# Kernel tuning notes

Measured on AMD Instinct MI355X. Metric: run time of the kernel, lower is better.

## Reference

```python
import jax, jax.numpy as jnp
import numpy as np

N_SAMPLES = 2 ** 15          # 32768
STEP = 256                   # transform_step_size
WIN = 2048                   # transform/synthesis window
N_FRAMES = N_SAMPLES // STEP # 128
N_COEFFS = WIN // 2 + 1      # 1025
DILATIONS = (1, 2, 4, 8, 16, 32, 64, 1)


def hann(n):
    return 0.5 - 0.5 * jnp.cos(2.0 * jnp.pi * jnp.arange(n, dtype=jnp.float32) / n)


def transform(audio):
    # audio: (B, 1, N) -> magnitude STFT (B, 1024, 128)
    x = audio[:, 0, :]
    x = jnp.pad(x, ((0, 0), (0, WIN - STEP)))  # pad so n_frames == N_SAMPLES // STEP
    idx = np.arange(N_FRAMES)[:, None] * STEP + np.arange(WIN)[None, :]
    frames = x[:, idx] * hann(WIN)
    spec = jnp.abs(jnp.fft.rfft(frames, norm='ortho'))   # (B, F, 1025)
    return spec[..., : N_COEFFS - 1].transpose(0, 2, 1)  # (B, 1024, F)


def conv1x1(x, w, b):
    # x: (B, I, T), w: (O, I, 1), b: (O,)
    return jnp.einsum('oi,bit->bot', w[:, :, 0], x) + b[None, :, None]


def anticausal_block(x, w, b, dilation):
    # kernel_size=2 anti-causal dilated conv: looks at t and t+dilation (pad future)
    x_fut = jnp.pad(x, ((0, 0), (0, 0), (0, dilation)))[:, :, dilation:]
    y = (jnp.einsum('oi,bit->bot', w[:, :, 0], x)
         + jnp.einsum('oi,bit->bot', w[:, :, 1], x_fut)
         + b[None, :, None])
    y = jax.nn.leaky_relu(y, 0.2)
    y = y + x
    # do_norm: per-example max-norm
    y = y / (jnp.max(jnp.abs(y), axis=(1, 2), keepdims=True) + 1e-8)
    return y


def upsample_with_holes(x, desired_size):
    # zero-stuffing upsample: out[..., ::step] = x
    b, c, t = x.shape
    step = desired_size // t
    out = jnp.zeros((b, c, desired_size), x.dtype)
    return out.at[:, :, ::step].set(x)


def freq_domain_resonance(coeffs):
    # coeffs: (1, C, 1025) in [0, 1); per-frame decay = repeated spectral multiply
    c = jnp.clip(coeffs, 0.0, 0.9999)
    exps = jnp.arange(1, N_FRAMES + 1, dtype=coeffs.dtype)
    mags = c[:, :, None, :] ** exps[None, None, :, None]     # (1, C, F, 1025)
    frames = jnp.fft.irfft(mags, n=WIN) * hann(WIN)
    hop = WIN // 2
    total = hop * (N_FRAMES - 1) + WIN
    idx = np.arange(N_FRAMES)[:, None] * hop + np.arange(WIN)[None, :]
    out = jnp.zeros(frames.shape[:2] + (total,), frames.dtype)
    out = out.at[:, :, idx].add(frames)                      # overlap-add
    return out[..., :N_SAMPLES]                              # (1, C, N)


def fft_convolve(a, b):
    # circular-free conv via zero-padding to 2N, keep first N (matches repo fft_convolve)
    n = a.shape[-1]
    spec = jnp.fft.rfft(a, n=2 * n) * jnp.fft.rfft(b, n=2 * n)
    return jnp.fft.irfft(spec, n=2 * n)[..., :n]


def reference(audio, proj_in_w, proj_in_b, blocks_w, blocks_b,
              proj_sparse_w, proj_sparse_b, proj_dense_w, proj_dense_b, resonances):
    spec = transform(audio)                         # (B, 1024, 128)
    h = conv1x1(spec, proj_in_w, proj_in_b)         # (B, 32, 128)
    acc = jnp.zeros_like(h)
    for i, d in enumerate(DILATIONS):               # fixed 8-block stack
        h = anticausal_block(h, blocks_w[i], blocks_b[i], d)
        acc = acc + h
    x = conv1x1(acc, proj_sparse_w, proj_sparse_b)  # (B, 256, 128)
    sparse = jax.nn.relu(x)
    x = conv1x1(sparse, proj_dense_w, proj_dense_b) # (B, 32, 128)
    x = upsample_with_holes(x, N_SAMPLES)           # (B, 32, 32768)
    res = freq_domain_resonance(resonances)         # (1, 32, 32768), broadcast over B
    y = fft_convolve(x, res)                        # (B, 32, 32768)
    y = jnp.sum(y, axis=1, keepdims=True)           # (B, 1, 32768)
    return y, sparse


def setup_inputs() -> dict:
    key = jax.random.key(0)
    ks = jax.random.split(key, 12)
    u = lambda k, shape: jax.random.uniform(k, shape, jnp.float32, -0.05, 0.05)
    return {
        'audio': jax.random.normal(ks[0], (32, 1, N_SAMPLES), jnp.float32),
        'proj_in_w': u(ks[1], (32, 1024, 1)),
        'proj_in_b': jnp.zeros((32,), jnp.float32),
        'blocks_w': u(ks[2], (8, 32, 32, 2)),
        'blocks_b': jnp.zeros((8, 32), jnp.float32),
        'proj_sparse_w': u(ks[3], (256, 32, 1)),
        'proj_sparse_b': jnp.zeros((256,), jnp.float32),
        'proj_dense_w': u(ks[4], (32, 256, 1)),
        'proj_dense_b': jnp.zeros((32,), jnp.float32),
        'resonances': jax.random.uniform(ks[5], (1, 32, N_COEFFS), jnp.float32, 0.0, 1.0),
    }
```

## Files before the change

### kernel.cpp

```cpp
#include <hip/hip_runtime.h>

#define PI_F 3.14159265358979323846f

typedef short bf16x8 __attribute__((ext_vector_type(8)));
typedef float f32x4 __attribute__((ext_vector_type(4)));

#define MFMA16(acc, a, b) \
  acc = __builtin_amdgcn_mfma_f32_16x16x32_bf16(a, b, acc, 0, 0, 0)

#define WS_SPEC   0u
#define WS_H0     4194304u
#define WS_ACC    4325376u
#define WS_V      4456448u
#define WS_WTIN   4587520u
#define WS_WST    4620288u
#define WS_WDT    4628480u
#define WS_FRAMES 4636672u
#define WS_RES    6733824u

#define BIX(a) ((a) + ((a) >> 4))

#define BFLY(I0, I1, C, S)                                   \
  { float2 u = buf[I0]; float2 w = buf[I1];                  \
    float tr = (C) * w.x - (S) * w.y;                        \
    float ti = (C) * w.y + (S) * w.x;                        \
    buf[I0] = make_float2(u.x + tr, u.y + ti);               \
    buf[I1] = make_float2(u.x - tr, u.y - ti); }

__device__ __forceinline__ void quad_bfly(float2* buf, int a, int h,
                                          float cs, float ss, float cp, float sp) {
  float2 x0 = buf[BIX(a)],         x1 = buf[BIX(a + h)];
  float2 x2 = buf[BIX(a + 2 * h)], x3 = buf[BIX(a + 3 * h)];
  float t1x = cs * x1.x - ss * x1.y, t1y = cs * x1.y + ss * x1.x;
  float t3x = cs * x3.x - ss * x3.y, t3y = cs * x3.y + ss * x3.x;
  float2 y0 = make_float2(x0.x + t1x, x0.y + t1y);
  float2 y1 = make_float2(x0.x - t1x, x0.y - t1y);
  float2 y2 = make_float2(x2.x + t3x, x2.y + t3y);
  float2 y3 = make_float2(x2.x - t3x, x2.y - t3y);
  float u2x = cp * y2.x - sp * y2.y, u2y = cp * y2.y + sp * y2.x;
  float u3x = sp * y3.x + cp * y3.y, u3y = sp * y3.y - cp * y3.x;
  buf[BIX(a)]         = make_float2(y0.x + u2x, y0.y + u2y);
  buf[BIX(a + 2 * h)] = make_float2(y0.x - u2x, y0.y - u2y);
  buf[BIX(a + h)]     = make_float2(y1.x + u3x, y1.y + u3y);
  buf[BIX(a + 3 * h)] = make_float2(y1.x - u3x, y1.y - u3y);
}

__device__ __forceinline__ void fft2048_stages(float2* buf, int tid) {
  const float R = 0.7071067811865476f;
  for (int g = tid; g < 512; g += 256) {
    int a = g << 2;
    float2 x0 = buf[BIX(a)],     x1 = buf[BIX(a + 1)];
    float2 x2 = buf[BIX(a + 2)], x3 = buf[BIX(a + 3)];
    float2 y0 = make_float2(x0.x + x1.x, x0.y + x1.y);
    float2 y1 = make_float2(x0.x - x1.x, x0.y - x1.y);
    float2 y2 = make_float2(x2.x + x3.x, x2.y + x3.y);
    float2 y3 = make_float2(x2.x - x3.x, x2.y - x3.y);
    buf[BIX(a)]     = make_float2(y0.x + y2.x, y0.y + y2.y);
    buf[BIX(a + 2)] = make_float2(y0.x - y2.x, y0.y - y2.y);
    buf[BIX(a + 1)] = make_float2(y1.x + y3.y, y1.y - y3.x);
    buf[BIX(a + 3)] = make_float2(y1.x - y3.y, y1.y + y3.x);
  }
  __syncthreads();
  {
    int j = tid & 3;
    const float C8 = 0.9238795325112867f, S8 = 0.3826834323650898f;
    float cs = (j == 0) ? 1.f : ((j == 1) ? R : ((j == 2) ? 0.f : -R));
    float ss = (j == 0) ? 0.f : ((j == 2) ? -1.f : -R);
    float cp = (j == 0) ? 1.f : ((j == 1) ? C8 : ((j == 2) ? R : S8));
    float sp = (j == 0) ? 0.f : ((j == 1) ? -S8 : ((j == 2) ? -R : -C8));
    for (int g = tid; g < 512; g += 256) {
      int a = ((g >> 2) << 4) + j;
      quad_bfly(buf, a, 4, cs, ss, cp, sp);
    }
  }
  __syncthreads();
#pragma unroll
  for (int s = 4; s <= 8; s += 2) {
    int h = 1 << s;
    int j = tid & (h - 1);
    float ss, cs, sp, cp;
    __sincosf(-PI_F / (float)h * (float)j, &ss, &cs);
    __sincosf(-PI_F / (float)(2 * h) * (float)j, &sp, &cp);
    for (int g = tid; g < 512; g += 256) {
      int a = ((g >> s) << (s + 2)) + j;
      quad_bfly(buf, a, h, cs, ss, cp, sp);
    }
    __syncthreads();
  }
  {
    float s0, c0;
    __sincosf(-PI_F / 1024.f * (float)tid, &s0, &c0);
    BFLY(BIX(tid),       BIX(tid + 1024), c0, s0);
    BFLY(BIX(tid + 256), BIX(tid + 1280), R * (c0 + s0), R * (s0 - c0));
    BFLY(BIX(tid + 512), BIX(tid + 1536), s0, -c0);
    BFLY(BIX(tid + 768), BIX(tid + 1792), R * (s0 - c0), -R * (s0 + c0));
  }
  __syncthreads();
}

__global__ __launch_bounds__(256) void k_fft(const float* __restrict__ audio,
                                             const float* __restrict__ resin,
                                             const float* __restrict__ Win,
                                             const float* __restrict__ Ws,
                                             const float* __restrict__ Wd,
                                             const float* __restrict__ bwIn,
                                             float* __restrict__ spec,
                                             float* __restrict__ frames,
                                             float* __restrict__ WT,
                                             float* __restrict__ WsT,
                                             float* __restrict__ WdT,
                                             short* __restrict__ Whg,
                                             short* __restrict__ Wlg) {
  __shared__ float2 buf[2176];
  int blk = blockIdx.x;

  if (blk >= 2560) {
    int i = (blk - 2560) * 256 + threadIdx.x;
    if (i < 32768) { int o = i >> 10, k = i & 1023; WT[k * 32 + o] = Win[i]; }
    if (i < 8192)  { int o2 = i >> 5, m = i & 31;   WsT[m * 256 + o2] = Ws[i]; }
    if (i < 8192)  { int c = i >> 8, o2 = i & 255;  WdT[o2 * 32 + c] = Wd[i]; }
    if (i < 16384) {
      int w = i & 1, m = (i >> 1) & 31, o = (i >> 6) & 31, s = i >> 11;
      float val = bwIn[i];
      unsigned bits = __float_as_uint(val);
      float rem = val - __uint_as_float(bits & 0xffff0000u);
      int row = (s * 2 + w) * 32 + o;
      Whg[row * 32 + m] = (short)(bits >> 16);
      Wlg[row * 32 + m] = (short)(__float_as_uint(rem) >> 16);
    }
    return;
  }

  if (blk < 2048) {
    int b  = blk >> 6;
    int f0 = (blk & 63) * 2;
    for (int j = threadIdx.x; j < 2048; j += 256) {
      float h = 0.5f - 0.5f * __cosf(0.0030679615757712823f * (float)j);
      int i1 = f0 * 256 + j;
      int i2 = i1 + 256;
      float a1 = (i1 < 32768) ? audio[b * 32768 + i1] : 0.f;
      float a2 = (i2 < 32768) ? audio[b * 32768 + i2] : 0.f;
      buf[BIX(__brev((unsigned)j) >> 21)] = make_float2(a1 * h, a2 * h);
    }
    __syncthreads();
    fft2048_stages(buf, threadIdx.x);
    const float scale = 0.5f * 0.022097086912079608f;
    for (int k = threadIdx.x; k < 1024; k += 256) {
      float2 zk = buf[BIX(k)];
      float2 zn = buf[BIX((2048 - k) & 2047)];
      float f1r = zk.x + zn.x, f1i = zk.y - zn.y;
      float f2r = zk.y + zn.y, f2i = zk.x - zn.x;
      spec[(b * 128 + f0) * 1024 + k]     = sqrtf(f1r * f1r + f1i * f1i) * scale;
      spec[(b * 128 + f0 + 1) * 1024 + k] = sqrtf(f2r * f2r + f2i * f2i) * scale;
    }
  } else {
    int r = blk - 2048;
    int c = r >> 4;
    int g = r & 15;
    float e1 = (float)(2 * g + 1);
    for (int k = threadIdx.x; k < 2048; k += 256) {
      int kk = (k <= 1024) ? k : 2048 - k;
      float cv = resin[c * 1025 + kk];
      cv = fminf(fmaxf(cv, 0.f), 0.9999f);
      float m1 = __powf(cv, e1);
      float m2 = m1 * cv;
      buf[BIX(__brev((unsigned)k) >> 21)] = make_float2(m1, m2);
    }
    __syncthreads();
    fft2048_stages(buf, threadIdx.x);
    for (int j = threadIdx.x; j < 2048; j += 256) {
      float h  = 0.5f - 0.5f * __cosf(0.0030679615757712823f * (float)j);
      float sc = h * (1.f / 2048.f);
      float2 z = buf[BIX(j)];
      frames[(c * 32 + 2 * g) * 2048 + j]     = z.x * sc;
      frames[(c * 32 + 2 * g + 1) * 2048 + j] = z.y * sc;
    }
  }
}

__global__ __launch_bounds__(256) void k_proj_in(const float* __restrict__ spec,
                                                 const float* __restrict__ WT,
                                                 const float* __restrict__ bias,
                                                 float* __restrict__ h0) {
  __shared__ float specL[8][1024];
  __shared__ float red[32][8][8];
  int b  = blockIdx.x >> 4;
  int t0 = (blockIdx.x & 15) * 8;
  for (int i = threadIdx.x; i < 8192; i += 256) {
    int tt = i >> 10, k = i & 1023;
    specL[tt][k] = spec[(b * 128 + t0 + tt) * 1024 + k];
  }
  __syncthreads();
  int o = threadIdx.x & 31, p = threadIdx.x >> 5;
  float part[8] = {0.f,0.f,0.f,0.f,0.f,0.f,0.f,0.f};
  for (int i = 0; i < 128; ++i) {
    int k = p * 128 + ((i + p * 4) & 127);
    float w = WT[k * 32 + o];
#pragma unroll
    for (int tt = 0; tt < 8; ++tt) part[tt] += w * specL[tt][k];
  }
#pragma unroll
  for (int tt = 0; tt < 8; ++tt) red[o][tt][p] = part[tt];
  __syncthreads();
  int oo = threadIdx.x >> 3, tt2 = threadIdx.x & 7;
  float s = bias[oo];
#pragma unroll
  for (int p2 = 0; p2 < 8; ++p2) s += red[oo][tt2][p2];
  h0[b * 4096 + oo * 128 + t0 + tt2] = s;
}

__global__ __launch_bounds__(256) void k_obpack(const float* __restrict__ frames,
                                                short* __restrict__ Bh,
                                                short* __restrict__ Bl) {
  int c = blockIdx.x >> 4, o = blockIdx.x & 15;
  int r = threadIdx.x;
  bf16x8 hv, lv;
#pragma unroll
  for (int j = 0; j < 8; ++j) {
    int fo = 8 * o + j;
    int g  = fo >> 2;
    int j0 = ((fo & 3) << 8) + r;
    float val = frames[(c * 32 + g) * 2048 + j0];
    if (g > 0) val += frames[(c * 32 + g - 1) * 2048 + j0 + 1024];
    unsigned bits = __float_as_uint(val);
    float rem = val - __uint_as_float(bits & 0xffff0000u);
    hv[j] = (short)(bits >> 16);
    lv[j] = (short)(__float_as_uint(rem) >> 16);
  }
  int unit = (blockIdx.x * 16 + (r >> 4)) * 16 + (r & 15);
  ((bf16x8*)Bh)[unit] = hv;
  ((bf16x8*)Bl)[unit] = lv;
}

__global__ __launch_bounds__(1024) void k_chain(const float* __restrict__ h0,
                                                const short* __restrict__ Whg,
                                                const short* __restrict__ Wlg,
                                                const float* __restrict__ bb,
                                                float* __restrict__ accout) {
  __shared__ __align__(16) short Hh[192 * 40];
  __shared__ __align__(16) short Hl[192 * 40];
  __shared__ float Hf[128 * 33];
  __shared__ float bL[256];
  __shared__ float red[16];
  int b = blockIdx.x, tid = threadIdx.x;

  for (int i = tid; i < 4096; i += 1024) {
    int t = i & 127;
    int o = i >> 7;
    float val = h0[b * 4096 + i];
    Hf[t * 33 + o] = val;
    unsigned bits = __float_as_uint(val);
    float rem = val - __uint_as_float(bits & 0xffff0000u);
    Hh[t * 40 + o] = (short)(bits >> 16);
    Hl[t * 40 + o] = (short)(__float_as_uint(rem) >> 16);
  }
  for (int i = tid; i < 64 * 40; i += 1024) {
    Hh[128 * 40 + i] = 0;
    Hl[128 * 40 + i] = 0;
  }
  if (tid < 256) bL[tid] = bb[tid];
  __syncthreads();

  int wave = tid >> 6, lane = tid & 63;
  int quad = lane >> 4, l15 = lane & 15;
  int t0 = (wave & 7) * 16, o0 = (wave >> 3) * 16;
  int tD = t0 + quad * 4;
  int oD = o0 + l15;

  const bf16x8* Hh8 = (const bf16x8*)Hh;
  const bf16x8* Hl8 = (const bf16x8*)Hl;
  const bf16x8* Wh8 = (const bf16x8*)Whg;
  const bf16x8* Wl8 = (const bf16x8*)Wlg;

  float accsum[4] = {0.f, 0.f, 0.f, 0.f};
  const int DIL[8] = {1, 2, 4, 8, 16, 32, 64, 1};

#pragma unroll
  for (int s = 0; s < 8; ++s) {
    int arow = t0 + l15;
    int frow = arow + DIL[s];
    bf16x8 Ah = Hh8[arow * 5 + quad];
    bf16x8 Al = Hl8[arow * 5 + quad];
    bf16x8 Fh = Hh8[frow * 5 + quad];
    bf16x8 Fl = Hl8[frow * 5 + quad];
    int w0row = ((s * 2 + 0) * 32 + oD) * 4 + quad;
    int w1row = ((s * 2 + 1) * 32 + oD) * 4 + quad;
    bf16x8 B0h = Wh8[w0row], B0l = Wl8[w0row];
    bf16x8 B1h = Wh8[w1row], B1l = Wl8[w1row];
    float bias = bL[s * 32 + oD];
    f32x4 acc = {bias, bias, bias, bias};
    MFMA16(acc, Ah, B0h); MFMA16(acc, Ah, B0l); MFMA16(acc, Al, B0h);
    MFMA16(acc, Fh, B1h); MFMA16(acc, Fh, B1l); MFMA16(acc, Fl, B1h);
    float hnew[4], lmax = 0.f;
#pragma unroll
    for (int r = 0; r < 4; ++r) {
      float sv = acc[r];
      sv = (sv > 0.f) ? sv : 0.2f * sv;
      sv += Hf[(tD + r) * 33 + oD];
      hnew[r] = sv;
      lmax = fmaxf(lmax, fabsf(sv));
    }
#pragma unroll
    for (int off = 32; off > 0; off >>= 1)
      lmax = fmaxf(lmax, __shfl_down(lmax, off, 64));
    if (lane == 0) red[wave] = lmax;
    __syncthreads();
    float mx = red[0];
#pragma unroll
    for (int i = 1; i < 16; ++i) mx = fmaxf(mx, red[i]);
    float nm = 1.f / (mx + 1e-8f);
#pragma unroll
    for (int r = 0; r < 4; ++r) {
      float hv = hnew[r] * nm;
      accsum[r] += hv;
      int t = tD + r;
      Hf[t * 33 + oD] = hv;
      unsigned bits = __float_as_uint(hv);
      float rem = hv - __uint_as_float(bits & 0xffff0000u);
      Hh[t * 40 + oD] = (short)(bits >> 16);
      Hl[t * 40 + oD] = (short)(__float_as_uint(rem) >> 16);
    }
    __syncthreads();
  }
#pragma unroll
  for (int r = 0; r < 4; ++r)
    accout[b * 4096 + (tD + r) * 32 + oD] = accsum[r];
}

__global__ __launch_bounds__(256) void k_sparse_dense(const float* __restrict__ acc,
                                                      const float* __restrict__ WsT,
                                                      const float* __restrict__ bs,
                                                      const float* __restrict__ WdT,
                                                      const float* __restrict__ bd,
                                                      float* __restrict__ out_sparse,
                                                      float* __restrict__ v) {
  __shared__ float accL[4][32];
  __shared__ float sL[4][256];
  __shared__ float red[8][4][32];
  int b = blockIdx.x >> 5, tq = blockIdx.x & 31;
  int t0 = tq * 4;
  int tid = threadIdx.x;
  if (tid < 128)
    accL[tid >> 5][tid & 31] = acc[b * 4096 + (t0 + (tid >> 5)) * 32 + (tid & 31)];
  __syncthreads();
  float bsv = bs[tid];
  float s0 = bsv, s1 = bsv, s2 = bsv, s3 = bsv;
  for (int m = 0; m < 32; ++m) {
    float w = WsT[m * 256 + tid];
    s0 += w * accL[0][m]; s1 += w * accL[1][m];
    s2 += w * accL[2][m]; s3 += w * accL[3][m];
  }
  s0 = fmaxf(s0, 0.f); s1 = fmaxf(s1, 0.f); s2 = fmaxf(s2, 0.f); s3 = fmaxf(s3, 0.f);
  float* os = out_sparse + b * 32768 + tid * 128 + t0;
  os[0] = s0; os[1] = s1; os[2] = s2; os[3] = s3;
  sL[0][tid] = s0; sL[1][tid] = s1; sL[2][tid] = s2; sL[3][tid] = s3;
  __syncthreads();
  int c = tid & 31, p = tid >> 5;
  float p0 = 0.f, p1 = 0.f, p2 = 0.f, p3 = 0.f;
  for (int jj = 0; jj < 32; ++jj) {
    int o2 = p * 32 + jj;
    float w = WdT[o2 * 32 + c];
    p0 += w * sL[0][o2]; p1 += w * sL[1][o2];
    p2 += w * sL[2][o2]; p3 += w * sL[3][o2];
  }
  red[p][0][c] = p0; red[p][1][c] = p1; red[p][2][c] = p2; red[p][3][c] = p3;
  __syncthreads();
  if (tid < 128) {
    int tt = tid >> 5, cc = tid & 31;
    float vv = bd[cc];
#pragma unroll
    for (int p2i = 0; p2i < 8; ++p2i) vv += red[p2i][tt][cc];
    v[b * 4096 + cc * 128 + t0 + tt] = vv;
  }
}

__global__ __launch_bounds__(512, 4) void k_conv(const float* __restrict__ v,
                                                 const short* __restrict__ Bh,
                                                 const short* __restrict__ Bl,
                                                 float* __restrict__ y) {
  __shared__ __align__(16) short AH[32 * 264];
  __shared__ __align__(16) short AL[32 * 264];
  __shared__ float vwin[2][16][48];

  int xcd  = blockIdx.x & 7;
  int slot = blockIdx.x >> 3;
  int e, b;
  if      (slot < 32) { e = xcd;      b = slot; }
  else if (slot < 64) { e = xcd + 8;  b = slot - 32; }
  else                { e = (xcd < 4) ? (xcd + 16) : (xcd + 12);
                        b = (xcd < 4) ? (slot - 64) : (slot - 48); }
  int j, uc;
  if      (e < 2)  { j = 0; uc = e; }
  else if (e < 6)  { j = 1; uc = e - 2; }
  else if (e < 12) { j = 2; uc = e - 6; }
  else             { j = 3; uc = e - 12; }
  int D0 = 32 * j - 16 * uc;

  for (int i = threadIdx.x; i < 1504; i += 512) {
    int ii = i % 47;
    int r  = i / 47;
    int c  = r & 15, ph = r >> 4;
    int d  = D0 - 15 + ii;
    vwin[ph][c][ii] = (d >= 0 && d < 128)
        ? v[b * 4096 + (16 * ph + c) * 128 + d] : 0.f;
  }
  __syncthreads();

  int lane = threadIdx.x & 63, wave = threadIdx.x >> 6;
  int quad = lane >> 4, l15 = lane & 15;
  int cq   = quad >> 1;
  int og   = 2 * uc + (quad & 1);
  int nt0  = wave * 2;

  f32x4 acc00 = (f32x4)0.f, acc01 = (f32x4)0.f;
  f32x4 acc10 = (f32x4)0.f, acc11 = (f32x4)0.f;

  const bf16x8* AH8 = (const bf16x8*)AH;
  const bf16x8* AL8 = (const bf16x8*)AL;
  const bf16x8* Bh8 = (const bf16x8*)Bh;
  const bf16x8* Bl8 = (const bf16x8*)Bl;
  short2* AH2 = (short2*)AH;
  short2* AL2 = (short2*)AL;

  int abase0 = (0 * 16 + l15) * 33 + quad;
  int abase1 = (1 * 16 + l15) * 33 + quad;

  for (int p = 0; p < 2; ++p) {
    for (int i = threadIdx.x; i < 4096; i += 512) {
      int kk2 = i & 127;
      int row = i >> 7;
      int cl  = kk2 >> 3;
      int uu  = (kk2 & 7) * 2;
      int ii  = row - uu + 15;
      float v0 = vwin[p][cl][ii];
      float v1 = vwin[p][cl][ii - 1];
      unsigned w0 = __float_as_uint(v0), w1 = __float_as_uint(v1);
      float r0 = v0 - __uint_as_float(w0 & 0xffff0000u);
      float r1 = v1 - __uint_as_float(w1 & 0xffff0000u);
      int u2 = row * 132 + kk2;
      AH2[u2] = make_short2((short)(w0 >> 16), (short)(w1 >> 16));
      AL2[u2] = make_short2((short)(__float_as_uint(r0) >> 16),
                            (short)(__float_as_uint(r1) >> 16));
    }
    __syncthreads();

#pragma unroll
    for (int ks = 0; ks < 8; ++ks) {
      bf16x8 ah0 = AH8[abase0 + ks * 4];
      bf16x8 al0 = AL8[abase0 + ks * 4];
      bf16x8 ah1 = AH8[abase1 + ks * 4];
      bf16x8 al1 = AL8[abase1 + ks * 4];
      int c   = 16 * p + 2 * ks + cq;
      int bb0 = (c * 16 + og) * 256 + l15;
      bf16x8 bh0 = Bh8[bb0 + nt0 * 16];
      bf16x8 bl0 = Bl8[bb0 + nt0 * 16];
      bf16x8 bh1 = Bh8[bb0 + (nt0 + 1) * 16];
      bf16x8 bl1 = Bl8[bb0 + (nt0 + 1) * 16];
      MFMA16(acc00, ah0, bh0); MFMA16(acc00, ah0, bl0); MFMA16(acc00, al0, bh0);
      MFMA16(acc10, ah1, bh0); MFMA16(acc10, ah1, bl0); MFMA16(acc10, al1, bh0);
      MFMA16(acc01, ah0, bh1); MFMA16(acc01, ah0, bl1); MFMA16(acc01, al0, bh1);
      MFMA16(acc11, ah1, bh1); MFMA16(acc11, ah1, bl1); MFMA16(acc11, al1, bh1);
    }
    __syncthreads();
  }

  {
    float* yb0 = y + b * 32768 + (32 * j + 0 * 16 + quad * 4) * 256 + l15;
    float* yb1 = y + b * 32768 + (32 * j + 1 * 16 + quad * 4) * 256 + l15;
#pragma unroll
    for (int reg = 0; reg < 4; ++reg) {
      atomicAdd(yb0 + reg * 256 + (nt0 + 0) * 16, acc00[reg]);
      atomicAdd(yb0 + reg * 256 + (nt0 + 1) * 16, acc01[reg]);
      atomicAdd(yb1 + reg * 256 + (nt0 + 0) * 16, acc10[reg]);
      atomicAdd(yb1 + reg * 256 + (nt0 + 1) * 16, acc11[reg]);
    }
  }
}

extern "C" void kernel_launch(void* const* d_in, const int* in_sizes, int n_in,
                              void* d_out, int out_size, void* d_ws, size_t ws_size,
                              hipStream_t stream) {
  const float* audio = (const float*)d_in[0];
  const float* Win   = (const float*)d_in[1];
  const float* bin   = (const float*)d_in[2];
  const float* bw    = (const float*)d_in[3];
  const float* bb    = (const float*)d_in[4];
  const float* Ws    = (const float*)d_in[5];
  const float* bs    = (const float*)d_in[6];
  const float* Wd    = (const float*)d_in[7];
  const float* bd    = (const float*)d_in[8];
  const float* reson = (const float*)d_in[9];

  float* out = (float*)d_out;
  float* ws  = (float*)d_ws;

  float* spec   = ws + WS_SPEC;
  float* h0     = ws + WS_H0;
  float* accb   = ws + WS_ACC;
  float* vbuf   = ws + WS_V;
  float* WT     = ws + WS_WTIN;
  float* WsT    = ws + WS_WST;
  float* WdT    = ws + WS_WDT;
  float* frames = ws + WS_FRAMES;
  short* Bh = (short*)(ws + WS_RES);
  short* Bl = (short*)(ws + WS_RES + 524288u);
  short* Whg = (short*)(ws + WS_V);
  short* Wlg = (short*)(ws + WS_V + 8192u);

  hipMemsetAsync(d_out, 0, 1048576u * sizeof(float), stream);

  k_fft<<<2688, 256, 0, stream>>>(audio, reson, Win, Ws, Wd, bw,
                                  spec, frames, WT, WsT, WdT, Whg, Wlg);
  k_obpack<<<512, 256, 0, stream>>>(frames, Bh, Bl);
  k_proj_in<<<512, 256, 0, stream>>>(spec, WT, bin, h0);
  k_chain<<<32, 1024, 0, stream>>>(h0, Whg, Wlg, bb, accb);
  k_sparse_dense<<<1024, 256, 0, stream>>>(accb, WsT, bs, WdT, bd, out + 1048576, vbuf);
  k_conv<<<640, 512, 0, stream>>>(vbuf, Bh, Bl, out);
}
```

Before: 181.3 us.

## Use radix-8 FFT stages and vectorized untransposed weights in proj_in

```diff
diff --git a/kernel.cpp b/kernel.cpp
--- a/kernel.cpp
+++ b/kernel.cpp
@@ -26,6 +26,9 @@
     float ti = (C) * w.y + (S) * w.x;                        \
     buf[I0] = make_float2(u.x + tr, u.y + ti);               \
     buf[I1] = make_float2(u.x - tr, u.y - ti); }
+
+#define CMULV(RX, RY, C, S, W) \
+  { RX = (C) * (W).x - (S) * (W).y; RY = (C) * (W).y + (S) * (W).x; }
 
 __device__ __forceinline__ void quad_bfly(float2* buf, int a, int h,
                                           float cs, float ss, float cp, float sp) {
@@ -45,55 +48,73 @@
   buf[BIX(a + 3 * h)] = make_float2(y1.x - u3x, y1.y - u3y);
 }
 
+__device__ __forceinline__ void octet_bfly(float2* buf, int a, int h,
+                                           float cv, float sv) {
+  const float R = 0.7071067811865476f;
+  float c1 = cv * cv - sv * sv, s1 = 2.f * cv * sv;
+  float c2 = c1 * c1 - s1 * s1, s2 = 2.f * c1 * s1;
+  float2 x0 = buf[BIX(a)],         x1 = buf[BIX(a + h)];
+  float2 x2 = buf[BIX(a + 2 * h)], x3 = buf[BIX(a + 3 * h)];
+  float2 x4 = buf[BIX(a + 4 * h)], x5 = buf[BIX(a + 5 * h)];
+  float2 x6 = buf[BIX(a + 6 * h)], x7 = buf[BIX(a + 7 * h)];
+  float tx, ty;
+  CMULV(tx, ty, c2, s2, x1);
+  float2 y0 = make_float2(x0.x + tx, x0.y + ty), y1 = make_float2(x0.x - tx, x0.y - ty);
+  CMULV(tx, ty, c2, s2, x3);
+  float2 y2 = make_float2(x2.x + tx, x2.y + ty), y3 = make_float2(x2.x - tx, x2.y - ty);
+  CMULV(tx, ty, c2, s2, x5);
+  float2 y4 = make_float2(x4.x + tx, x4.y + ty), y5 = make_float2(x4.x - tx, x4.y - ty);
+  CMULV(tx, ty, c2, s2, x7);
+  float2 y6 = make_float2(x6.x + tx, x6.y + ty), y7 = make_float2(x6.x - tx, x6.y - ty);
+  CMULV(tx, ty, c1, s1, y2);
+  float2 z0 = make_float2(y0.x + tx, y0.y + ty), z2 = make_float2(y0.x - tx, y0.y - ty);
+  CMULV(tx, ty, c1, s1, y3);
+  float2 z1 = make_float2(y1.x + ty, y1.y - tx), z3 = make_float2(y1.x - ty, y1.y + tx);
+  CMULV(tx, ty, c1, s1, y6);
+  float2 z4 = make_float2(y4.x + tx, y4.y + ty), z6 = make_float2(y4.x - tx, y4.y - ty);
+  CMULV(tx, ty, c1, s1, y7);
+  float2 z5 = make_float2(y5.x + ty, y5.y - tx), z7 = make_float2(y5.x - ty, y5.y + tx);
+  float ca = R * (cv + sv), sa = R * (sv - cv);
+  float cb = sv,            sb = -cv;
+  float cc = R * (sv - cv), sc = -R * (cv + sv);
+  CMULV(tx, ty, cv, sv, z4);
+  buf[BIX(a)]         = make_float2(z0.x + tx, z0.y + ty);
+  buf[BIX(a + 4 * h)] = make_float2(z0.x - tx, z0.y - ty);
+  CMULV(tx, ty, ca, sa, z5);
+  buf[BIX(a + h)]     = make_float2(z1.x + tx, z1.y + ty);
+  buf[BIX(a + 5 * h)] = make_float2(z1.x - tx, z1.y - ty);
+  CMULV(tx, ty, cb, sb, z6);
+  buf[BIX(a + 2 * h)] = make_float2(z2.x + tx, z2.y + ty);
+  buf[BIX(a + 6 * h)] = make_float2(z2.x - tx, z2.y - ty);
+  CMULV(tx, ty, cc, sc, z7);
+  buf[BIX(a + 3 * h)] = make_float2(z3.x + tx, z3.y + ty);
+  buf[BIX(a + 7 * h)] = make_float2(z3.x - tx, z3.y - ty);
+}
+
 __device__ __forceinline__ void fft2048_stages(float2* buf, int tid) {
-  const float R = 0.7071067811865476f;
+  octet_bfly(buf, tid << 3, 1, 1.f, 0.f);
+  __syncthreads();
+  {
+    int j = tid & 7;
+    int a = ((tid >> 3) << 6) + j;
+    float sv, cv;
+    __sincosf(-PI_F / 32.f * (float)j, &sv, &cv);
+    octet_bfly(buf, a, 8, cv, sv);
+  }
+  __syncthreads();
+  {
+    int j = tid & 63;
+    int a = ((tid >> 6) << 9) + j;
+    float sv, cv;
+    __sincosf(-PI_F / 256.f * (float)j, &sv, &cv);
+    octet_bfly(buf, a, 64, cv, sv);
+  }
+  __syncthreads();
   for (int g = tid; g < 512; g += 256) {
-    int a = g << 2;
-    float2 x0 = buf[BIX(a)],     x1 = buf[BIX(a + 1)];
-    float2 x2 = buf[BIX(a + 2)], x3 = buf[BIX(a + 3)];
-    float2 y0 = make_float2(x0.x + x1.x, x0.y + x1.y);
-    float2 y1 = make_float2(x0.x - x1.x, x0.y - x1.y);
-    float2 y2 = make_float2(x2.x + x3.x, x2.y + x3.y);
-    float2 y3 = make_float2(x2.x - x3.x, x2.y - x3.y);
-    buf[BIX(a)]     = make_float2(y0.x + y2.x, y0.y + y2.y);
-    buf[BIX(a + 2)] = make_float2(y0.x - y2.x, y0.y - y2.y);
-    buf[BIX(a + 1)] = make_float2(y1.x + y3.y, y1.y - y3.x);
-    buf[BIX(a + 3)] = make_float2(y1.x - y3.y, y1.y + y3.x);
-  }
-  __syncthreads();
-  {
-    int j = tid & 3;
-    const float C8 = 0.9238795325112867f, S8 = 0.3826834323650898f;
-    float cs = (j == 0) ? 1.f : ((j == 1) ? R : ((j == 2) ? 0.f : -R));
-    float ss = (j == 0) ? 0.f : ((j == 2) ? -1.f : -R);
-    float cp = (j == 0) ? 1.f : ((j == 1) ? C8 : ((j == 2) ? R : S8));
-    float sp = (j == 0) ? 0.f : ((j == 1) ? -S8 : ((j == 2) ? -R : -C8));
-    for (int g = tid; g < 512; g += 256) {
-      int a = ((g >> 2) << 4) + j;
-      quad_bfly(buf, a, 4, cs, ss, cp, sp);
-    }
-  }
-  __syncthreads();
-#pragma unroll
-  for (int s = 4; s <= 8; s += 2) {
-    int h = 1 << s;
-    int j = tid & (h - 1);
-    float ss, cs, sp, cp;
-    __sincosf(-PI_F / (float)h * (float)j, &ss, &cs);
-    __sincosf(-PI_F / (float)(2 * h) * (float)j, &sp, &cp);
-    for (int g = tid; g < 512; g += 256) {
-      int a = ((g >> s) << (s + 2)) + j;
-      quad_bfly(buf, a, h, cs, ss, cp, sp);
-    }
-    __syncthreads();
-  }
-  {
-    float s0, c0;
-    __sincosf(-PI_F / 1024.f * (float)tid, &s0, &c0);
-    BFLY(BIX(tid),       BIX(tid + 1024), c0, s0);
-    BFLY(BIX(tid + 256), BIX(tid + 1280), R * (c0 + s0), R * (s0 - c0));
-    BFLY(BIX(tid + 512), BIX(tid + 1536), s0, -c0);
-    BFLY(BIX(tid + 768), BIX(tid + 1792), R * (s0 - c0), -R * (s0 + c0));
+    float sp, cp;
+    __sincosf(-PI_F / 1024.f * (float)g, &sp, &cp);
+    float c2 = cp * cp - sp * sp, s2 = 2.f * cp * sp;
+    quad_bfly(buf, g, 512, c2, s2, cp, sp);
   }
   __syncthreads();
 }
@@ -179,7 +200,7 @@
 }
 
 __global__ __launch_bounds__(256) void k_proj_in(const float* __restrict__ spec,
-                                                 const float* __restrict__ WT,
+                                                 const float* __restrict__ Win,
                                                  const float* __restrict__ bias,
                                                  float* __restrict__ h0) {
   __shared__ float specL[8][1024];
@@ -193,11 +214,15 @@
   __syncthreads();
   int o = threadIdx.x & 31, p = threadIdx.x >> 5;
   float part[8] = {0.f,0.f,0.f,0.f,0.f,0.f,0.f,0.f};
-  for (int i = 0; i < 128; ++i) {
-    int k = p * 128 + ((i + p * 4) & 127);
-    float w = WT[k * 32 + o];
-#pragma unroll
-    for (int tt = 0; tt < 8; ++tt) part[tt] += w * specL[tt][k];
+  const float4* Wrow = (const float4*)(Win + o * 1024);
+  for (int k4 = p * 32; k4 < p * 32 + 32; ++k4) {
+    float4 w4 = Wrow[k4];
+    int k = k4 * 4;
+#pragma unroll
+    for (int tt = 0; tt < 8; ++tt) {
+      float4 s4 = *(const float4*)&specL[tt][k];
+      part[tt] += w4.x * s4.x + w4.y * s4.y + w4.z * s4.z + w4.w * s4.w;
+    }
   }
 #pragma unroll
   for (int tt = 0; tt < 8; ++tt) red[o][tt][p] = part[tt];
@@ -512,7 +537,7 @@
   k_fft<<<2688, 256, 0, stream>>>(audio, reson, Win, Ws, Wd, bw,
                                   spec, frames, WT, WsT, WdT, Whg, Wlg);
   k_obpack<<<512, 256, 0, stream>>>(frames, Bh, Bl);
-  k_proj_in<<<512, 256, 0, stream>>>(spec, WT, bin, h0);
+  k_proj_in<<<512, 256, 0, stream>>>(spec, Win, bin, h0);
   k_chain<<<32, 1024, 0, stream>>>(h0, Whg, Wlg, bb, accb);
   k_sparse_dense<<<1024, 256, 0, stream>>>(accb, WsT, bs, WdT, bd, out + 1048576, vbuf);
   k_conv<<<640, 512, 0, stream>>>(vbuf, Bh, Bl, out);
```

Result: faster. 177.6 us (-2.0%).
